# Kernel tuning notes

Hardware: AMD Instinct MI355X
Metric: run time of the kernel (lower is better)

Reference implementation:

```python
import math
import jax, jax.numpy as jnp
import numpy as np

B, N, D, H, L = 8, 1024, 512, 8, 6
HD = D // H
FREQ = 256
K_LORENTZ = 1.0


def lorentz_projx(x, k=K_LORENTZ):
    # geoopt Lorentz.projx: x0 = sqrt(k + ||x_space||^2)
    space = x[..., 1:]
    x0 = jnp.sqrt(k + jnp.sum(space * space, axis=-1, keepdims=True))
    return jnp.concatenate([x0, space], axis=-1)


def layernorm(x, eps=1e-6):
    m = jnp.mean(x, axis=-1, keepdims=True)
    v = jnp.mean((x - m) ** 2, axis=-1, keepdims=True)
    return (x - m) / jnp.sqrt(v + eps)


def make_pe(n, d):
    pos = np.arange(n, dtype=np.float32)[:, None]
    div = np.exp(np.arange(0, d, 2, dtype=np.float32) * (-math.log(10000.0) / d))
    pe = np.zeros((n, d), dtype=np.float32)
    pe[:, 0::2] = np.sin(pos * div)
    pe[:, 1::2] = np.cos(pos * div)
    return jnp.asarray(pe)


def setup_inputs() -> dict:
    key = jax.random.key(0)
    ks = jax.random.split(key, 20)
    s = 0.02
    inp = {
        "t": jax.random.uniform(ks[0], (B,), jnp.float32) * 1000.0,
        "x": jax.random.normal(ks[1], (B, N, D), jnp.float32),
        "mask": jnp.ones((B, N), jnp.float32),
        "pe": make_pe(N, D),
        # timestep embedder MLP (weights stored [in,out])
        "tw1": jax.random.normal(ks[2], (FREQ, D), jnp.float32) * s,
        "tb1": jnp.zeros((D,), jnp.float32),
        "tw2": jax.random.normal(ks[3], (D, D), jnp.float32) * s,
        "tb2": jnp.zeros((D,), jnp.float32),
        # per-layer params stacked over L
        "Wq": jax.random.normal(ks[4], (L, D, D), jnp.float32) * s,
        "bq": jnp.zeros((L, D), jnp.float32),
        "Wk": jax.random.normal(ks[5], (L, D, D), jnp.float32) * s,
        "bk": jnp.zeros((L, D), jnp.float32),
        "Wv": jax.random.normal(ks[6], (L, D, D), jnp.float32) * s,
        "bv": jnp.zeros((L, D), jnp.float32),
        "W1": jax.random.normal(ks[7], (L, D, 4 * D), jnp.float32) * s,
        "b1": jnp.zeros((L, 4 * D), jnp.float32),
        "W2": jax.random.normal(ks[8], (L, 4 * D, D), jnp.float32) * s,
        "b2": jnp.zeros((L, D), jnp.float32),
        "Wada": jax.random.normal(ks[9], (L, D, 6 * D), jnp.float32) * s,
        "bada": jnp.zeros((L, 6 * D), jnp.float32),
    }
    return inp


def timestep_embedding(t, dim=FREQ, max_period=10000.0):
    half = dim // 2
    freqs = jnp.exp(-math.log(max_period) * jnp.arange(half, dtype=jnp.float32) / half)
    args = t[:, None] * freqs[None]
    return jnp.concatenate([jnp.cos(args), jnp.sin(args)], axis=-1)  # [B, dim]


def attention(h, mask, Wq, bq, Wk, bk, Wv, bv):
    # h: [B,N,D], mask: [B,N]
    q = (h @ Wq + bq).reshape(B, N, H, HD).transpose(0, 2, 1, 3)
    k = (h @ Wk + bk).reshape(B, N, H, HD).transpose(0, 2, 1, 3)
    v = (h @ Wv + bv).reshape(B, N, H, HD).transpose(0, 2, 1, 3)
    scores = jnp.einsum("bhqd,bhkd->bhqk", q, k) / math.sqrt(HD)
    # faithful quirk: valid positions get +1 added, invalid get -10000
    mm = jnp.einsum("bi,bj->bij", mask, mask)[:, None]  # [B,1,N,N]
    mm = jnp.where(mm == 0, -10000.0, mm)
    scores = scores + mm
    probs = jax.nn.softmax(scores, axis=-1)
    ctx = jnp.einsum("bhqk,bhkd->bhqd", probs, v)
    return ctx.transpose(0, 2, 1, 3).reshape(B, N, D)


def reference(t, x, mask, pe, tw1, tb1, tw2, tb2, Wq, bq, Wk, bk, Wv, bv,
              W1, b1, W2, b2, Wada, bada):
    # z = x + PositionalEncoding(x) = 2*x + pe
    z = x + (x + pe[None])
    # timestep embedder
    c = timestep_embedding(t) @ tw1 + tb1
    c = jax.nn.silu(c) @ tw2 + tb2  # [B, D]
    for i in range(L):
        ada = jax.nn.silu(c) @ Wada[i] + bada[i]  # [B, 6D]
        sh_msa, sc_msa, g_msa, sh_mlp, sc_mlp, g_mlp = jnp.split(ada, 6, axis=-1)
        h = layernorm(z) * (1.0 + sc_msa[:, None]) + sh_msa[:, None]
        z = z + g_msa[:, None] * attention(h, mask, Wq[i], bq[i], Wk[i], bk[i], Wv[i], bv[i])
        z = lorentz_projx(z)
        h = layernorm(z) * (1.0 + sc_mlp[:, None]) + sh_mlp[:, None]
        m = jax.nn.gelu(h @ W1[i] + b1[i], approximate=True) @ W2[i] + b2[i]
        z = z + g_mlp[:, None] * m
        z = lorentz_projx(z)
    z = lorentz_projx(z)
    return jnp.where(mask[:, :, None] != 0, z, 0.0)
```

## Files before the change

### kernel.cpp

```cpp
#include <hip/hip_runtime.h>
#include <hip/hip_bf16.h>
#include <math.h>

#define NTOK 1024
#define DMODEL 512
#define NHEAD 8
#define HDIM 64
#define BATCH 8
#define NLAYER 6
#define ROWS (BATCH*NTOK)
#define QKVSTR 1536
#define LOG2E 1.44269504f

typedef __attribute__((ext_vector_type(8))) short bf16x8;
typedef __attribute__((ext_vector_type(4))) float f32x4;
typedef unsigned short ushort_t;


__device__ __forceinline__ float silu_f(float x) { return x / (1.f + expf(-x)); }

__device__ __forceinline__ float gelu_tanh_f(float x) {
    float x3 = x * x * x;
    float y2 = 1.5957691216057308f * (x + 0.044715f * x3);
    float e = __builtin_amdgcn_exp2f(-y2 * LOG2E);
    return x / (1.f + e);
}

__device__ __forceinline__ unsigned short f2bf(float x) {
    __hip_bfloat16 b = __float2bfloat16(x);
    return *reinterpret_cast<unsigned short*>(&b);
}

__device__ __forceinline__ float bf2f(unsigned short u) {
    union { float f; unsigned v; } c;
    c.v = (unsigned)u << 16;
    return c.f;
}

template<int NW>
__device__ __forceinline__ float blk_sum(float v, volatile float* scratch) {
    #pragma unroll
    for (int o = 32; o > 0; o >>= 1) v += __shfl_down(v, o);
    if ((threadIdx.x & 63) == 0) scratch[threadIdx.x >> 6] = v;
    __syncthreads();
    float s = scratch[0];
    #pragma unroll
    for (int i = 1; i < NW; i++) s += scratch[i];
    __syncthreads();
    return s;
}


__global__ __launch_bounds__(256) void init_z_kernel(const float* __restrict__ x,
                                                     const float* __restrict__ pe,
                                                     float* __restrict__ z) {
    int i = blockIdx.x * 256 + threadIdx.x;
    const int C4 = DMODEL / 4;
    int row = i / C4;
    int col4 = i - row * C4;
    int n = row & (NTOK - 1);
    float4 xv = ((const float4*)x)[i];
    float4 pv = ((const float4*)pe)[n * C4 + col4];
    float4 o;
    o.x = 2.f * xv.x + pv.x;
    o.y = 2.f * xv.y + pv.y;
    o.z = 2.f * xv.z + pv.z;
    o.w = 2.f * xv.w + pv.w;
    ((float4*)z)[i] = o;
}

__global__ void temb_kernel(const float* __restrict__ t, float* __restrict__ temb) {
    int b = blockIdx.x;
    int j = threadIdx.x;
    float f = expf(-9.210340371976184f * (float)j / 128.f);
    float a = t[b] * f;
    temb[b * 256 + j] = cosf(a);
    temb[b * 256 + 128 + j] = sinf(a);
}

__global__ __launch_bounds__(256) void skinny_part(const float* __restrict__ A,
                                                   const float* __restrict__ W,
                                                   float* __restrict__ part,
                                                   int K, int N, int NL) {
    __shared__ float Als[8][128];
    const int l = blockIdx.z;
    const int n = blockIdx.x * 256 + threadIdx.x;
    const int kc = blockIdx.y;
    const int kbase = kc * 128;
    for (int i = threadIdx.x; i < 8 * 128; i += 256) {
        int b = i >> 7, k = i & 127;
        Als[b][k] = A[b * K + kbase + k];
    }
    __syncthreads();
    float acc[8] = {};
    const float* wp = W + (size_t)l * K * N + (size_t)kbase * N + n;
    for (int k = 0; k < 128; k += 4) {
        float w0 = wp[0];
        float w1 = wp[N];
        float w2 = wp[2 * N];
        float w3 = wp[3 * N];
        wp += 4 * (size_t)N;
        #pragma unroll
        for (int b = 0; b < 8; b++)
            acc[b] += Als[b][k] * w0 + Als[b][k + 1] * w1 + Als[b][k + 2] * w2 + Als[b][k + 3] * w3;
    }
    #pragma unroll
    for (int b = 0; b < 8; b++)
        part[((size_t)kc * 8 + b) * NL + (size_t)l * N + n] = acc[b];
}

template<int ACT>
__global__ __launch_bounds__(256) void skinny_reduce(const float* __restrict__ part,
                                                     const float* __restrict__ bias,
                                                     float* __restrict__ out,
                                                     int KC, int N, int NL) {
    int i = blockIdx.x * 256 + threadIdx.x;
    if (i >= 8 * NL) return;
    int b = i / NL, n = i - b * NL;
    float s = bias[n];
    for (int kc = 0; kc < KC; kc++) s += part[((size_t)kc * 8 + b) * NL + n];
    if (ACT == 1) s = silu_f(s);
    int l = n / N, nl = n - l * N;
    out[((size_t)l * 8 + b) * N + nl] = s;
}

__global__ __launch_bounds__(256) void transp_all(const float* __restrict__ Wq,
                                                  const float* __restrict__ Wk,
                                                  const float* __restrict__ Wv,
                                                  const float* __restrict__ W1,
                                                  const float* __restrict__ W2,
                                                  ushort_t* __restrict__ wqkv_t,
                                                  ushort_t* __restrict__ w1_t,
                                                  ushort_t* __restrict__ w2_t) {
    __shared__ float tile[32][33];
    int blk = blockIdx.x;
    const float* src; ushort_t* dst; int K, N, k0, n0;
    if (blk < 768) {
        int zz = blk >> 8, rem = blk & 255;
        k0 = (rem >> 4) * 32; n0 = (rem & 15) * 32;
        src = zz == 0 ? Wq : (zz == 1 ? Wk : Wv);
        dst = wqkv_t + zz * 512 * 512;
        K = 512; N = 512;
    } else if (blk < 1792) {
        int rem = blk - 768;
        n0 = (rem & 63) * 32; k0 = (rem >> 6) * 32;
        src = W1; dst = w1_t; K = 512; N = 2048;
    } else {
        int rem = blk - 1792;
        n0 = (rem & 15) * 32; k0 = (rem >> 4) * 32;
        src = W2; dst = w2_t; K = 2048; N = 512;
    }
    int c = threadIdx.x & 31, r8 = threadIdx.x >> 5;
    #pragma unroll
    for (int i = 0; i < 4; i++) {
        int r = r8 + i * 8;
        tile[r][c] = src[(size_t)(k0 + r) * N + n0 + c];
    }
    __syncthreads();
    #pragma unroll
    for (int i = 0; i < 4; i++) {
        int rr = r8 + i * 8;
        dst[(size_t)(n0 + rr) * K + k0 + c] = f2bf(tile[c][rr]);
    }
}

__global__ void pack_bias(const float* __restrict__ bq, const float* __restrict__ bk,
                          const float* __restrict__ bv, float* __restrict__ bqkv) {
    int idx = blockIdx.x * 256 + threadIdx.x;
    if (idx >= NLAYER * QKVSTR) return;
    int l = idx / QKVSTR, n = idx - l * QKVSTR;
    float v = (n < 512) ? bq[l * 512 + n] : (n < 1024) ? bk[l * 512 + n - 512] : bv[l * 512 + n - 1024];
    bqkv[idx] = v;
}

template<int ACT, int OUTBF, int QPRESCALE>
__global__ __launch_bounds__(256) void mfma_gemm(const ushort_t* __restrict__ A,
                                                 const ushort_t* __restrict__ Bt,
                                                 const float* __restrict__ bias,
                                                 void* __restrict__ Cout,
                                                 int M, int N, int K) {
    __shared__ ushort_t smem[4 * 128 * 64];
    const int tid = threadIdx.x;
    const int lane = tid & 63, wv = tid >> 6;
    const int wm = (wv >> 1) * 64, wn = (wv & 1) * 64;
    const int lrow = lane & 15, lk = lane >> 4;
    const int m0 = blockIdx.x * 128, n0 = blockIdx.y * 128;
    const int srow = lane >> 3;
    const int qp = lane & 7;
    const int ql = qp ^ srow;

    f32x4 acc[4][4];
    #pragma unroll
    for (int i = 0; i < 4; i++)
        #pragma unroll
        for (int j = 0; j < 4; j++) {
            f32x4 zz = {0.f, 0.f, 0.f, 0.f};
            acc[i][j] = zz;
        }

    const int nK = K >> 6;

    auto STAGE = [&](int p, int ks) {
        const int k0 = ks << 6;
        ushort_t* Ad = smem + p * 8192;
        ushort_t* Bd = smem + 16384 + p * 8192;
        #pragma unroll
        for (int it = 0; it < 4; it++) {
            int chunk = wv * 4 + it;
            int row = chunk * 8 + srow;
            const ushort_t* srcA = A + (size_t)(m0 + row) * K + k0 + ql * 8;
            const ushort_t* srcB = Bt + (size_t)(n0 + row) * K + k0 + ql * 8;
            __builtin_amdgcn_global_load_lds((const __attribute__((address_space(1))) void*)srcA,
                                             (__attribute__((address_space(3))) void*)(Ad + chunk * 512),
                                             16, 0, 0);
            __builtin_amdgcn_global_load_lds((const __attribute__((address_space(1))) void*)srcB,
                                             (__attribute__((address_space(3))) void*)(Bd + chunk * 512),
                                             16, 0, 0);
        }
    };

    STAGE(0, 0);
    int cur = 0;
    for (int ks = 0; ks < nK; ks++) {
        if (ks + 1 < nK) {
            STAGE(cur ^ 1, ks + 1);
            asm volatile("s_waitcnt vmcnt(8)" ::: "memory");
        } else {
            asm volatile("s_waitcnt vmcnt(0)" ::: "memory");
        }
        __builtin_amdgcn_s_barrier();
        asm volatile("" ::: "memory");

        const ushort_t* Ab = smem + cur * 8192;
        const ushort_t* Bb = smem + 16384 + cur * 8192;
        #pragma unroll
        for (int kk = 0; kk < 2; kk++) {
            bf16x8 af[4], bfr[4];
            #pragma unroll
            for (int f = 0; f < 4; f++) {
                int ar = wm + f * 16 + lrow;
                af[f] = *(const bf16x8*)(Ab + ar * 64 + (((kk * 4 + lk) ^ (ar & 7)) << 3));
                int br = wn + f * 16 + lrow;
                bfr[f] = *(const bf16x8*)(Bb + br * 64 + (((kk * 4 + lk) ^ (br & 7)) << 3));
            }
            #pragma unroll
            for (int i = 0; i < 4; i++)
                #pragma unroll
                for (int j = 0; j < 4; j++)
                    acc[i][j] = __builtin_amdgcn_mfma_f32_16x16x32_bf16(af[i], bfr[j], acc[i][j], 0, 0, 0);
        }
        asm volatile("" ::: "memory");
        __builtin_amdgcn_s_barrier();
        cur ^= 1;
    }

    if (OUTBF) {
        __syncthreads();
        #pragma unroll
        for (int j = 0; j < 4; j++) {
            int coll = wn + j * 16 + lrow;
            float bcol = bias[n0 + coll];
            #pragma unroll
            for (int i = 0; i < 4; i++) {
                #pragma unroll
                for (int r = 0; r < 4; r++) {
                    int rowl = wm + i * 16 + lk * 4 + r;
                    float v = acc[i][j][r] + bcol;
                    if (ACT == 1) v = gelu_tanh_f(v);
                    if (QPRESCALE && (n0 + coll) < 512) v *= 0.125f * LOG2E;
                    smem[rowl * 136 + coll] = f2bf(v);
                }
            }
        }
        __syncthreads();
        ushort_t* Co = (ushort_t*)Cout;
        #pragma unroll
        for (int pass = 0; pass < 8; pass++) {
            int rowl = pass * 16 + (tid >> 4);
            int cseg = (tid & 15) * 8;
            uint4 vv = *(const uint4*)(smem + rowl * 136 + cseg);
            *(uint4*)(Co + (size_t)(m0 + rowl) * N + n0 + cseg) = vv;
        }
    } else {
        #pragma unroll
        for (int j = 0; j < 4; j++) {
            int col = n0 + wn + j * 16 + lrow;
            float bcol = bias[col];
            #pragma unroll
            for (int i = 0; i < 4; i++)
                #pragma unroll
                for (int r = 0; r < 4; r++) {
                    int row = m0 + wm + i * 16 + lk * 4 + r;
                    float v = acc[i][j][r] + bcol;
                    if (ACT == 1) v = gelu_tanh_f(v);
                    ((float*)Cout)[(size_t)row * N + col] = v;
                }
        }
    }
}


__global__ __launch_bounds__(128) void ln_mod_kernel(const float* __restrict__ z,
                                                     const float* __restrict__ ada,
                                                     ushort_t* __restrict__ out,
                                                     int sh_off, int sc_off) {
    __shared__ float red[2];
    int row = blockIdx.x;
    int b = row >> 10;
    int tid = threadIdx.x;
    float4 v = ((const float4*)(z + (size_t)row * DMODEL))[tid];
    float s = v.x + v.y + v.z + v.w;
    float mean = blk_sum<2>(s, red) * (1.f / DMODEL);
    float dx = v.x - mean, dy = v.y - mean, dz = v.z - mean, dw = v.w - mean;
    float ssq = dx * dx + dy * dy + dz * dz + dw * dw;
    float var = blk_sum<2>(ssq, red) * (1.f / DMODEL);
    float rstd = rsqrtf(var + 1e-6f);
    const float* ab = ada + b * (6 * DMODEL);
    float4 sc4 = ((const float4*)(ab + sc_off))[tid];
    float4 sh4 = ((const float4*)(ab + sh_off))[tid];
    unsigned short u0 = f2bf(dx * rstd * (1.f + sc4.x) + sh4.x);
    unsigned short u1 = f2bf(dy * rstd * (1.f + sc4.y) + sh4.y);
    unsigned short u2 = f2bf(dz * rstd * (1.f + sc4.z) + sh4.z);
    unsigned short u3 = f2bf(dw * rstd * (1.f + sc4.w) + sh4.w);
    uint2 pk;
    pk.x = (unsigned)u0 | ((unsigned)u1 << 16);
    pk.y = (unsigned)u2 | ((unsigned)u3 << 16);
    ((uint2*)(out + (size_t)row * DMODEL))[tid] = pk;
}

__global__ __launch_bounds__(128) void resid_ln_kernel(float* __restrict__ z,
                                                       const ushort_t* __restrict__ add,
                                                       const float* __restrict__ adaG, int g_off,
                                                       const float* __restrict__ adaLN, int sh_off, int sc_off,
                                                       ushort_t* __restrict__ out) {
    __shared__ float red[2];
    int row = blockIdx.x;
    int b = row >> 10;
    int tid = threadIdx.x;
    float4 v = ((float4*)(z + (size_t)row * DMODEL))[tid];
    uint2 a2 = ((const uint2*)(add + (size_t)row * DMODEL))[tid];
    float4 g4 = ((const float4*)(adaG + b * (6 * DMODEL) + g_off))[tid];
    v.x += g4.x * bf2f((unsigned short)(a2.x & 0xffff));
    v.y += g4.y * bf2f((unsigned short)(a2.x >> 16));
    v.z += g4.z * bf2f((unsigned short)(a2.y & 0xffff));
    v.w += g4.w * bf2f((unsigned short)(a2.y >> 16));
    float ssq = v.x * v.x + v.y * v.y + v.z * v.z + v.w * v.w;
    if (tid == 0) ssq -= v.x * v.x;
    float tot = blk_sum<2>(ssq, red);
    if (tid == 0) v.x = sqrtf(1.f + tot);
    ((float4*)(z + (size_t)row * DMODEL))[tid] = v;
    float s = v.x + v.y + v.z + v.w;
    float mean = blk_sum<2>(s, red) * (1.f / DMODEL);
    float dx = v.x - mean, dy = v.y - mean, dz = v.z - mean, dw = v.w - mean;
    float sq2 = dx * dx + dy * dy + dz * dz + dw * dw;
    float var = blk_sum<2>(sq2, red) * (1.f / DMODEL);
    float rstd = rsqrtf(var + 1e-6f);
    const float* ab = adaLN + b * (6 * DMODEL);
    float4 sc4 = ((const float4*)(ab + sc_off))[tid];
    float4 sh4 = ((const float4*)(ab + sh_off))[tid];
    unsigned short u0 = f2bf(dx * rstd * (1.f + sc4.x) + sh4.x);
    unsigned short u1 = f2bf(dy * rstd * (1.f + sc4.y) + sh4.y);
    unsigned short u2 = f2bf(dz * rstd * (1.f + sc4.z) + sh4.z);
    unsigned short u3 = f2bf(dw * rstd * (1.f + sc4.w) + sh4.w);
    uint2 pk;
    pk.x = (unsigned)u0 | ((unsigned)u1 << 16);
    pk.y = (unsigned)u2 | ((unsigned)u3 << 16);
    ((uint2*)(out + (size_t)row * DMODEL))[tid] = pk;
}

__global__ __launch_bounds__(128) void resid_final_kernel(const float* __restrict__ z,
                                                          const ushort_t* __restrict__ add,
                                                          const float* __restrict__ adaG, int g_off,
                                                          const float* __restrict__ mask,
                                                          float* __restrict__ out) {
    __shared__ float red[2];
    int row = blockIdx.x;
    int b = row >> 10;
    int tid = threadIdx.x;
    float4 v = ((const float4*)(z + (size_t)row * DMODEL))[tid];
    uint2 a2 = ((const uint2*)(add + (size_t)row * DMODEL))[tid];
    float4 g4 = ((const float4*)(adaG + b * (6 * DMODEL) + g_off))[tid];
    v.x += g4.x * bf2f((unsigned short)(a2.x & 0xffff));
    v.y += g4.y * bf2f((unsigned short)(a2.x >> 16));
    v.z += g4.z * bf2f((unsigned short)(a2.y & 0xffff));
    v.w += g4.w * bf2f((unsigned short)(a2.y >> 16));
    float ssq = v.x * v.x + v.y * v.y + v.z * v.z + v.w * v.w;
    if (tid == 0) ssq -= v.x * v.x;
    float tot = blk_sum<2>(ssq, red);
    if (tid == 0) v.x = sqrtf(1.f + tot);
    float m = mask[row];
    if (m == 0.f) { v.x = 0.f; v.y = 0.f; v.z = 0.f; v.w = 0.f; }
    ((float4*)(out + (size_t)row * DMODEL))[tid] = v;
}

__global__ __launch_bounds__(512) void flash_attn_mfma(const ushort_t* __restrict__ qkv,
                                                       const float* __restrict__ mask,
                                                       ushort_t* __restrict__ ctx) {
    __shared__ ushort_t Kls[64 * 64];
    __shared__ ushort_t Vt[64 * 64];
    __shared__ ushort_t Pls[8][16 * 64];
    __shared__ float Mall[NTOK];

    const int tid = threadIdx.x;
    const int lane = tid & 63, w = tid >> 6;
    const int c = lane & 15, g = lane >> 4;
    const int bh = blockIdx.x;
    const int q0 = blockIdx.y * 128;
    const int b = bh >> 3, h = bh & 7;

    const ushort_t* qptr = qkv + (size_t)(b * NTOK + q0 + w * 16 + c) * QKVSTR + h * HDIM + g * 8;
    bf16x8 aq0 = *(const bf16x8*)(qptr);
    bf16x8 aq1 = *(const bf16x8*)(qptr + 32);

    const float mq = mask[b * NTOK + q0 + w * 16 + c];

    #pragma unroll
    for (int i = 0; i < 2; i++) Mall[tid + i * 512] = mask[b * NTOK + tid + i * 512];

    f32x4 o[4];
    #pragma unroll
    for (int j = 0; j < 4; j++) { f32x4 zz = {0.f,0.f,0.f,0.f}; o[j] = zz; }
    float l_run = 0.f;

    const int srow = lane >> 3, qp = lane & 7, ql = qp ^ srow;
    const int kp = tid & 31, dg = tid >> 5;

    char* Pw = (char*)&Pls[w][0];
    const int cswz = (c & 7) << 4;

    for (int kt = 0; kt < NTOK / 64; kt++) {
        const int k0 = kt * 64;
        __syncthreads();
        {
            int row = w * 8 + srow;
            const ushort_t* src = qkv + (size_t)(b * NTOK + k0 + row) * QKVSTR + 512 + h * HDIM + ql * 8;
            __builtin_amdgcn_global_load_lds((const __attribute__((address_space(1))) void*)src,
                                             (__attribute__((address_space(3))) void*)(Kls + w * 512),
                                             16, 0, 0);
        }
        {
            const ushort_t* v0 = qkv + (size_t)(b * NTOK + k0 + 2 * kp) * QKVSTR + 1024 + h * HDIM + dg * 4;
            uint2 r0 = *(const uint2*)v0;
            uint2 r1 = *(const uint2*)(v0 + QKVSTR);
            const ushort_t* e0 = (const ushort_t*)&r0;
            const ushort_t* e1 = (const ushort_t*)&r1;
            unsigned* VtU = (unsigned*)Vt;
            #pragma unroll
            for (int i = 0; i < 4; i++) {
                int d = dg * 4 + i;
                unsigned pk = (unsigned)e0[i] | ((unsigned)e1[i] << 16);
                VtU[d * 32 + (((kp >> 2) ^ (d & 7)) << 2) + (kp & 3)] = pk;
            }
        }
        __syncthreads();

        f32x4 s[4];
        #pragma unroll
        for (int j = 0; j < 4; j++) { f32x4 zz = {0.f,0.f,0.f,0.f}; s[j] = zz; }
        __builtin_amdgcn_s_setprio(1);
        #pragma unroll
        for (int j = 0; j < 4; j++) {
            int row = j * 16 + c;
            bf16x8 ak0 = *(const bf16x8*)(Kls + row * 64 + ((g ^ (row & 7)) << 3));
            bf16x8 ak1 = *(const bf16x8*)(Kls + row * 64 + (((4 + g) ^ (row & 7)) << 3));
            s[j] = __builtin_amdgcn_mfma_f32_16x16x32_bf16(ak0, aq0, s[j], 0, 0, 0);
            s[j] = __builtin_amdgcn_mfma_f32_16x16x32_bf16(ak1, aq1, s[j], 0, 0, 0);
        }
        __builtin_amdgcn_s_setprio(0);

        #pragma unroll
        for (int j = 0; j < 4; j++) {
            float4 mk4 = *(const float4*)&Mall[k0 + j * 16 + 4 * g];
            const float* mkp = (const float*)&mk4;
            float p[4];
            #pragma unroll
            for (int r = 0; r < 4; r++) {
                float mm = mq * mkp[r];
                float sv = s[j][r] + (mm == 0.f ? -14427.0f : mm * LOG2E);
                p[r] = exp2f(sv);
                l_run += p[r];
            }
            uint2 pk2;
            pk2.x = (unsigned)f2bf(p[0]) | ((unsigned)f2bf(p[1]) << 16);
            pk2.y = (unsigned)f2bf(p[2]) | ((unsigned)f2bf(p[3]) << 16);
            *(uint2*)(Pw + c * 128 + ((j * 32 + g * 8) ^ cswz)) = pk2;
        }

        __builtin_amdgcn_s_setprio(1);
        #pragma unroll
        for (int kk = 0; kk < 2; kk++) {
            bf16x8 pa = *(const bf16x8*)(Pw + c * 128 + ((kk * 64 + g * 16) ^ cswz));
            #pragma unroll
            for (int j = 0; j < 4; j++) {
                int vr = j * 16 + c;
                bf16x8 bv = *(const bf16x8*)(Vt + vr * 64 + (((kk * 4 + g) ^ (vr & 7)) << 3));
                o[j] = __builtin_amdgcn_mfma_f32_16x16x32_bf16(pa, bv, o[j], 0, 0, 0);
            }
        }
        __builtin_amdgcn_s_setprio(0);
    }

    l_run += __shfl_xor(l_run, 16);
    l_run += __shfl_xor(l_run, 32);

    float invr[4];
    #pragma unroll
    for (int r = 0; r < 4; r++) invr[r] = 1.f / __shfl(l_run, (g << 4) + 4 * g + r);
    #pragma unroll
    for (int r = 0; r < 4; r++) {
        size_t row = (size_t)(b * NTOK + q0 + w * 16 + 4 * g + r) * DMODEL + h * HDIM;
        #pragma unroll
        for (int j = 0; j < 4; j++)
            ctx[row + j * 16 + c] = f2bf(o[j][r] * invr[r]);
    }
}


extern "C" void kernel_launch(void* const* d_in, const int* in_sizes, int n_in,
                              void* d_out, int out_size, void* d_ws, size_t ws_size,
                              hipStream_t stream) {
    const float* t    = (const float*)d_in[0];
    const float* x    = (const float*)d_in[1];
    const float* mask = (const float*)d_in[2];
    const float* pe   = (const float*)d_in[3];
    const float* tw1  = (const float*)d_in[4];
    const float* tb1  = (const float*)d_in[5];
    const float* tw2  = (const float*)d_in[6];
    const float* tb2  = (const float*)d_in[7];
    const float* Wq   = (const float*)d_in[8];
    const float* bq   = (const float*)d_in[9];
    const float* Wk   = (const float*)d_in[10];
    const float* bk   = (const float*)d_in[11];
    const float* Wv   = (const float*)d_in[12];
    const float* bv   = (const float*)d_in[13];
    const float* W1   = (const float*)d_in[14];
    const float* b1   = (const float*)d_in[15];
    const float* W2   = (const float*)d_in[16];
    const float* b2   = (const float*)d_in[17];
    const float* Wada = (const float*)d_in[18];
    const float* bada = (const float*)d_in[19];
    float* out = (float*)d_out;

    float* z      = (float*)d_ws;
    ushort_t* cxb = (ushort_t*)(z + (size_t)ROWS * DMODEL);
    ushort_t* qkv = cxb + (size_t)ROWS * DMODEL;
    ushort_t* mid = qkv;
    ushort_t* hb  = qkv + (size_t)ROWS * 2048;
    ushort_t* wqkv_t = hb + (size_t)ROWS * DMODEL;
    ushort_t* w1_t   = wqkv_t + 1536 * 512;
    ushort_t* w2_t   = w1_t + 2048 * 512;
    float* bqkv  = (float*)(w2_t + 512 * 2048);
    float* temb  = bqkv + NLAYER * QKVSTR;
    float* cmid  = temb + BATCH * 256;
    float* scs   = cmid + BATCH * DMODEL;
    float* part  = scs + BATCH * DMODEL;
    float* ada_all = part + 4 * 8 * (NLAYER * 3072);

    init_z_kernel<<<ROWS * DMODEL / 4 / 256, 256, 0, stream>>>(x, pe, z);
    temb_kernel<<<BATCH, 128, 0, stream>>>(t, temb);
    pack_bias<<<(NLAYER * QKVSTR + 255) / 256, 256, 0, stream>>>(bq, bk, bv, bqkv);

    skinny_part<<<dim3(2, 2, 1), 256, 0, stream>>>(temb, tw1, part, 256, 512, 512);
    skinny_reduce<1><<<16, 256, 0, stream>>>(part, tb1, cmid, 2, 512, 512);
    skinny_part<<<dim3(2, 4, 1), 256, 0, stream>>>(cmid, tw2, part, 512, 512, 512);
    skinny_reduce<1><<<16, 256, 0, stream>>>(part, tb2, scs, 4, 512, 512);
    skinny_part<<<dim3(12, 4, NLAYER), 256, 0, stream>>>(scs, Wada, part, 512, 3072, NLAYER * 3072);
    skinny_reduce<0><<<(8 * NLAYER * 3072 + 255) / 256, 256, 0, stream>>>(
        part, bada, ada_all, 4, 3072, NLAYER * 3072);

    dim3 gqkv(ROWS / 128, QKVSTR / 128);
    dim3 gmlp1(ROWS / 128, 2048 / 128);
    dim3 gmlp2(ROWS / 128, DMODEL / 128);
    dim3 ga(BATCH * NHEAD, NTOK / 128);

    ln_mod_kernel<<<ROWS, 128, 0, stream>>>(z, ada_all, hb, 0, 512);

    for (int i = 0; i < NLAYER; i++) {
        const float* ada = ada_all + (size_t)i * 8 * 3072;

        transp_all<<<2816, 256, 0, stream>>>(Wq + (size_t)i * 512 * 512,
                                             Wk + (size_t)i * 512 * 512,
                                             Wv + (size_t)i * 512 * 512,
                                             W1 + (size_t)i * 512 * 2048,
                                             W2 + (size_t)i * 2048 * 512,
                                             wqkv_t, w1_t, w2_t);

        mfma_gemm<0, 1, 1><<<gqkv, 256, 0, stream>>>(hb, wqkv_t, bqkv + i * QKVSTR, qkv,
                                                     ROWS, QKVSTR, DMODEL);

        flash_attn_mfma<<<ga, 512, 0, stream>>>(qkv, mask, cxb);

        resid_ln_kernel<<<ROWS, 128, 0, stream>>>(z, cxb, ada, 2 * DMODEL,
                                                  ada, 3 * DMODEL, 4 * DMODEL, hb);

        mfma_gemm<1, 1, 0><<<gmlp1, 256, 0, stream>>>(hb, w1_t, b1 + (size_t)i * 4 * DMODEL, mid,
                                                      ROWS, 4 * DMODEL, DMODEL);
        mfma_gemm<0, 1, 0><<<gmlp2, 256, 0, stream>>>(mid, w2_t, b2 + (size_t)i * DMODEL, cxb,
                                                      ROWS, DMODEL, 4 * DMODEL);

        if (i < NLAYER - 1) {
            const float* adan = ada_all + (size_t)(i + 1) * 8 * 3072;
            resid_ln_kernel<<<ROWS, 128, 0, stream>>>(z, cxb, ada, 5 * DMODEL,
                                                      adan, 0, 512, hb);
        } else {
            resid_final_kernel<<<ROWS, 128, 0, stream>>>(z, cxb, ada, 5 * DMODEL, mask, out);
        }
    }
}
```

Before: 928.6 us.

## Use one wave per row for LN kernels and shrink attention tiles to 64 queries

```diff
diff --git a/kernel.cpp b/kernel.cpp
--- a/kernel.cpp
+++ b/kernel.cpp
@@ -37,17 +37,10 @@
     return c.f;
 }
 
-template<int NW>
-__device__ __forceinline__ float blk_sum(float v, volatile float* scratch) {
-    #pragma unroll
-    for (int o = 32; o > 0; o >>= 1) v += __shfl_down(v, o);
-    if ((threadIdx.x & 63) == 0) scratch[threadIdx.x >> 6] = v;
-    __syncthreads();
-    float s = scratch[0];
-    #pragma unroll
-    for (int i = 1; i < NW; i++) s += scratch[i];
-    __syncthreads();
-    return s;
+__device__ __forceinline__ float wave_sum(float v) {
+    #pragma unroll
+    for (int o = 1; o < 64; o <<= 1) v += __shfl_xor(v, o);
+    return v;
 }
 
 
@@ -300,122 +293,140 @@
 }
 
 
-__global__ __launch_bounds__(128) void ln_mod_kernel(const float* __restrict__ z,
+__global__ __launch_bounds__(256) void ln_mod_kernel(const float* __restrict__ z,
                                                      const float* __restrict__ ada,
                                                      ushort_t* __restrict__ out,
                                                      int sh_off, int sc_off) {
-    __shared__ float red[2];
-    int row = blockIdx.x;
+    int lane = threadIdx.x & 63;
+    int row = blockIdx.x * 4 + (threadIdx.x >> 6);
     int b = row >> 10;
-    int tid = threadIdx.x;
-    float4 v = ((const float4*)(z + (size_t)row * DMODEL))[tid];
-    float s = v.x + v.y + v.z + v.w;
-    float mean = blk_sum<2>(s, red) * (1.f / DMODEL);
-    float dx = v.x - mean, dy = v.y - mean, dz = v.z - mean, dw = v.w - mean;
-    float ssq = dx * dx + dy * dy + dz * dz + dw * dw;
-    float var = blk_sum<2>(ssq, red) * (1.f / DMODEL);
-    float rstd = rsqrtf(var + 1e-6f);
+    const float4* zr = (const float4*)(z + (size_t)row * DMODEL);
+    float4 va = zr[lane * 2], vb = zr[lane * 2 + 1];
+    float s = va.x + va.y + va.z + va.w + vb.x + vb.y + vb.z + vb.w;
+    float mean = wave_sum(s) * (1.f / DMODEL);
+    float d0 = va.x - mean, d1 = va.y - mean, d2 = va.z - mean, d3 = va.w - mean;
+    float d4 = vb.x - mean, d5 = vb.y - mean, d6 = vb.z - mean, d7 = vb.w - mean;
+    float ssq = d0*d0 + d1*d1 + d2*d2 + d3*d3 + d4*d4 + d5*d5 + d6*d6 + d7*d7;
+    float rstd = rsqrtf(wave_sum(ssq) * (1.f / DMODEL) + 1e-6f);
     const float* ab = ada + b * (6 * DMODEL);
-    float4 sc4 = ((const float4*)(ab + sc_off))[tid];
-    float4 sh4 = ((const float4*)(ab + sh_off))[tid];
-    unsigned short u0 = f2bf(dx * rstd * (1.f + sc4.x) + sh4.x);
-    unsigned short u1 = f2bf(dy * rstd * (1.f + sc4.y) + sh4.y);
-    unsigned short u2 = f2bf(dz * rstd * (1.f + sc4.z) + sh4.z);
-    unsigned short u3 = f2bf(dw * rstd * (1.f + sc4.w) + sh4.w);
-    uint2 pk;
-    pk.x = (unsigned)u0 | ((unsigned)u1 << 16);
-    pk.y = (unsigned)u2 | ((unsigned)u3 << 16);
-    ((uint2*)(out + (size_t)row * DMODEL))[tid] = pk;
-}
-
-__global__ __launch_bounds__(128) void resid_ln_kernel(float* __restrict__ z,
+    const float4* scp = (const float4*)(ab + sc_off);
+    const float4* shp = (const float4*)(ab + sh_off);
+    float4 sca = scp[lane * 2], scb = scp[lane * 2 + 1];
+    float4 sha = shp[lane * 2], shb = shp[lane * 2 + 1];
+    uint4 pk;
+    pk.x = (unsigned)f2bf(d0 * rstd * (1.f + sca.x) + sha.x) |
+           ((unsigned)f2bf(d1 * rstd * (1.f + sca.y) + sha.y) << 16);
+    pk.y = (unsigned)f2bf(d2 * rstd * (1.f + sca.z) + sha.z) |
+           ((unsigned)f2bf(d3 * rstd * (1.f + sca.w) + sha.w) << 16);
+    pk.z = (unsigned)f2bf(d4 * rstd * (1.f + scb.x) + shb.x) |
+           ((unsigned)f2bf(d5 * rstd * (1.f + scb.y) + shb.y) << 16);
+    pk.w = (unsigned)f2bf(d6 * rstd * (1.f + scb.z) + shb.z) |
+           ((unsigned)f2bf(d7 * rstd * (1.f + scb.w) + shb.w) << 16);
+    ((uint4*)(out + (size_t)row * DMODEL))[lane] = pk;
+}
+
+__global__ __launch_bounds__(256) void resid_ln_kernel(float* __restrict__ z,
                                                        const ushort_t* __restrict__ add,
                                                        const float* __restrict__ adaG, int g_off,
                                                        const float* __restrict__ adaLN, int sh_off, int sc_off,
                                                        ushort_t* __restrict__ out) {
-    __shared__ float red[2];
-    int row = blockIdx.x;
+    int lane = threadIdx.x & 63;
+    int row = blockIdx.x * 4 + (threadIdx.x >> 6);
     int b = row >> 10;
-    int tid = threadIdx.x;
-    float4 v = ((float4*)(z + (size_t)row * DMODEL))[tid];
-    uint2 a2 = ((const uint2*)(add + (size_t)row * DMODEL))[tid];
-    float4 g4 = ((const float4*)(adaG + b * (6 * DMODEL) + g_off))[tid];
-    v.x += g4.x * bf2f((unsigned short)(a2.x & 0xffff));
-    v.y += g4.y * bf2f((unsigned short)(a2.x >> 16));
-    v.z += g4.z * bf2f((unsigned short)(a2.y & 0xffff));
-    v.w += g4.w * bf2f((unsigned short)(a2.y >> 16));
-    float ssq = v.x * v.x + v.y * v.y + v.z * v.z + v.w * v.w;
-    if (tid == 0) ssq -= v.x * v.x;
-    float tot = blk_sum<2>(ssq, red);
-    if (tid == 0) v.x = sqrtf(1.f + tot);
-    ((float4*)(z + (size_t)row * DMODEL))[tid] = v;
-    float s = v.x + v.y + v.z + v.w;
-    float mean = blk_sum<2>(s, red) * (1.f / DMODEL);
-    float dx = v.x - mean, dy = v.y - mean, dz = v.z - mean, dw = v.w - mean;
-    float sq2 = dx * dx + dy * dy + dz * dz + dw * dw;
-    float var = blk_sum<2>(sq2, red) * (1.f / DMODEL);
-    float rstd = rsqrtf(var + 1e-6f);
+    float4* zr = (float4*)(z + (size_t)row * DMODEL);
+    float4 va = zr[lane * 2], vb = zr[lane * 2 + 1];
+    uint4 a4 = ((const uint4*)(add + (size_t)row * DMODEL))[lane];
+    const float4* gp = (const float4*)(adaG + b * (6 * DMODEL) + g_off);
+    float4 ga = gp[lane * 2], gb = gp[lane * 2 + 1];
+    const ushort_t* e = (const ushort_t*)&a4;
+    va.x += ga.x * bf2f(e[0]); va.y += ga.y * bf2f(e[1]);
+    va.z += ga.z * bf2f(e[2]); va.w += ga.w * bf2f(e[3]);
+    vb.x += gb.x * bf2f(e[4]); vb.y += gb.y * bf2f(e[5]);
+    vb.z += gb.z * bf2f(e[6]); vb.w += gb.w * bf2f(e[7]);
+    float ssq = va.x*va.x + va.y*va.y + va.z*va.z + va.w*va.w
+              + vb.x*vb.x + vb.y*vb.y + vb.z*vb.z + vb.w*vb.w;
+    if (lane == 0) ssq -= va.x * va.x;
+    float tot = wave_sum(ssq);
+    if (lane == 0) va.x = sqrtf(1.f + tot);
+    zr[lane * 2] = va; zr[lane * 2 + 1] = vb;
+    float s = va.x + va.y + va.z + va.w + vb.x + vb.y + vb.z + vb.w;
+    float mean = wave_sum(s) * (1.f / DMODEL);
+    float d0 = va.x - mean, d1 = va.y - mean, d2 = va.z - mean, d3 = va.w - mean;
+    float d4 = vb.x - mean, d5 = vb.y - mean, d6 = vb.z - mean, d7 = vb.w - mean;
+    float sq2 = d0*d0 + d1*d1 + d2*d2 + d3*d3 + d4*d4 + d5*d5 + d6*d6 + d7*d7;
+    float rstd = rsqrtf(wave_sum(sq2) * (1.f / DMODEL) + 1e-6f);
     const float* ab = adaLN + b * (6 * DMODEL);
-    float4 sc4 = ((const float4*)(ab + sc_off))[tid];
-    float4 sh4 = ((const float4*)(ab + sh_off))[tid];
-    unsigned short u0 = f2bf(dx * rstd * (1.f + sc4.x) + sh4.x);
-    unsigned short u1 = f2bf(dy * rstd * (1.f + sc4.y) + sh4.y);
-    unsigned short u2 = f2bf(dz * rstd * (1.f + sc4.z) + sh4.z);
-    unsigned short u3 = f2bf(dw * rstd * (1.f + sc4.w) + sh4.w);
-    uint2 pk;
-    pk.x = (unsigned)u0 | ((unsigned)u1 << 16);
-    pk.y = (unsigned)u2 | ((unsigned)u3 << 16);
-    ((uint2*)(out + (size_t)row * DMODEL))[tid] = pk;
-}
-
-__global__ __launch_bounds__(128) void resid_final_kernel(const float* __restrict__ z,
+    const float4* scp = (const float4*)(ab + sc_off);
+    const float4* shp = (const float4*)(ab + sh_off);
+    float4 sca = scp[lane * 2], scb = scp[lane * 2 + 1];
+    float4 sha = shp[lane * 2], shb = shp[lane * 2 + 1];
+    uint4 pk;
+    pk.x = (unsigned)f2bf(d0 * rstd * (1.f + sca.x) + sha.x) |
+           ((unsigned)f2bf(d1 * rstd * (1.f + sca.y) + sha.y) << 16);
+    pk.y = (unsigned)f2bf(d2 * rstd * (1.f + sca.z) + sha.z) |
+           ((unsigned)f2bf(d3 * rstd * (1.f + sca.w) + sha.w) << 16);
+    pk.z = (unsigned)f2bf(d4 * rstd * (1.f + scb.x) + shb.x) |
+           ((unsigned)f2bf(d5 * rstd * (1.f + scb.y) + shb.y) << 16);
+    pk.w = (unsigned)f2bf(d6 * rstd * (1.f + scb.z) + shb.z) |
+           ((unsigned)f2bf(d7 * rstd * (1.f + scb.w) + shb.w) << 16);
+    ((uint4*)(out + (size_t)row * DMODEL))[lane] = pk;
+}
+
+__global__ __launch_bounds__(256) void resid_final_kernel(const float* __restrict__ z,
                                                           const ushort_t* __restrict__ add,
                                                           const float* __restrict__ adaG, int g_off,
                                                           const float* __restrict__ mask,
                                                           float* __restrict__ out) {
-    __shared__ float red[2];
-    int row = blockIdx.x;
+    int lane = threadIdx.x & 63;
+    int row = blockIdx.x * 4 + (threadIdx.x >> 6);
     int b = row >> 10;
-    int tid = threadIdx.x;
-    float4 v = ((const float4*)(z + (size_t)row * DMODEL))[tid];
-    uint2 a2 = ((const uint2*)(add + (size_t)row * DMODEL))[tid];
-    float4 g4 = ((const float4*)(adaG + b * (6 * DMODEL) + g_off))[tid];
-    v.x += g4.x * bf2f((unsigned short)(a2.x & 0xffff));
-    v.y += g4.y * bf2f((unsigned short)(a2.x >> 16));
-    v.z += g4.z * bf2f((unsigned short)(a2.y & 0xffff));
-    v.w += g4.w * bf2f((unsigned short)(a2.y >> 16));
-    float ssq = v.x * v.x + v.y * v.y + v.z * v.z + v.w * v.w;
-    if (tid == 0) ssq -= v.x * v.x;
-    float tot = blk_sum<2>(ssq, red);
-    if (tid == 0) v.x = sqrtf(1.f + tot);
+    const float4* zr = (const float4*)(z + (size_t)row * DMODEL);
+    float4 va = zr[lane * 2], vb = zr[lane * 2 + 1];
+    uint4 a4 = ((const uint4*)(add + (size_t)row * DMODEL))[lane];
+    const float4* gp = (const float4*)(adaG + b * (6 * DMODEL) + g_off);
+    float4 ga = gp[lane * 2], gb = gp[lane * 2 + 1];
+    const ushort_t* e = (const ushort_t*)&a4;
+    va.x += ga.x * bf2f(e[0]); va.y += ga.y * bf2f(e[1]);
+    va.z += ga.z * bf2f(e[2]); va.w += ga.w * bf2f(e[3]);
+    vb.x += gb.x * bf2f(e[4]); vb.y += gb.y * bf2f(e[5]);
+    vb.z += gb.z * bf2f(e[6]); vb.w += gb.w * bf2f(e[7]);
+    float ssq = va.x*va.x + va.y*va.y + va.z*va.z + va.w*va.w
+              + vb.x*vb.x + vb.y*vb.y + vb.z*vb.z + vb.w*vb.w;
+    if (lane == 0) ssq -= va.x * va.x;
+    float tot = wave_sum(ssq);
+    if (lane == 0) va.x = sqrtf(1.f + tot);
     float m = mask[row];
-    if (m == 0.f) { v.x = 0.f; v.y = 0.f; v.z = 0.f; v.w = 0.f; }
-    ((float4*)(out + (size_t)row * DMODEL))[tid] = v;
-}
-
-__global__ __launch_bounds__(512) void flash_attn_mfma(const ushort_t* __restrict__ qkv,
+    if (m == 0.f) {
+        va.x = va.y = va.z = va.w = 0.f;
+        vb.x = vb.y = vb.z = vb.w = 0.f;
+    }
+    float4* orow = (float4*)(out + (size_t)row * DMODEL);
+    orow[lane * 2] = va; orow[lane * 2 + 1] = vb;
+}
+
+__global__ __launch_bounds__(256) void flash_attn_mfma(const ushort_t* __restrict__ qkv,
                                                        const float* __restrict__ mask,
                                                        ushort_t* __restrict__ ctx) {
     __shared__ ushort_t Kls[64 * 64];
     __shared__ ushort_t Vt[64 * 64];
-    __shared__ ushort_t Pls[8][16 * 64];
+    __shared__ ushort_t Pls[4][16 * 64];
     __shared__ float Mall[NTOK];
 
     const int tid = threadIdx.x;
     const int lane = tid & 63, w = tid >> 6;
     const int c = lane & 15, g = lane >> 4;
     const int bh = blockIdx.x;
-    const int q0 = blockIdx.y * 128;
+    const int q0 = blockIdx.y * 64;
     const int b = bh >> 3, h = bh & 7;
 
     const ushort_t* qptr = qkv + (size_t)(b * NTOK + q0 + w * 16 + c) * QKVSTR + h * HDIM + g * 8;
     bf16x8 aq0 = *(const bf16x8*)(qptr);
     bf16x8 aq1 = *(const bf16x8*)(qptr + 32);
 
-    const float mq = mask[b * NTOK + q0 + w * 16 + c];
-
-    #pragma unroll
-    for (int i = 0; i < 2; i++) Mall[tid + i * 512] = mask[b * NTOK + tid + i * 512];
+    const float mqL = mask[b * NTOK + q0 + w * 16 + c] * LOG2E;
+
+    #pragma unroll
+    for (int i = 0; i < 4; i++) Mall[tid + i * 256] = mask[b * NTOK + tid + i * 256];
 
     f32x4 o[4];
     #pragma unroll
@@ -431,23 +442,25 @@
     for (int kt = 0; kt < NTOK / 64; kt++) {
         const int k0 = kt * 64;
         __syncthreads();
-        {
-            int row = w * 8 + srow;
+        #pragma unroll
+        for (int it = 0; it < 2; it++) {
+            int chunk = w * 2 + it;
+            int row = chunk * 8 + srow;
             const ushort_t* src = qkv + (size_t)(b * NTOK + k0 + row) * QKVSTR + 512 + h * HDIM + ql * 8;
             __builtin_amdgcn_global_load_lds((const __attribute__((address_space(1))) void*)src,
-                                             (__attribute__((address_space(3))) void*)(Kls + w * 512),
+                                             (__attribute__((address_space(3))) void*)(Kls + chunk * 512),
                                              16, 0, 0);
         }
         {
-            const ushort_t* v0 = qkv + (size_t)(b * NTOK + k0 + 2 * kp) * QKVSTR + 1024 + h * HDIM + dg * 4;
-            uint2 r0 = *(const uint2*)v0;
-            uint2 r1 = *(const uint2*)(v0 + QKVSTR);
+            const ushort_t* v0 = qkv + (size_t)(b * NTOK + k0 + 2 * kp) * QKVSTR + 1024 + h * HDIM + dg * 8;
+            uint4 r0 = *(const uint4*)v0;
+            uint4 r1 = *(const uint4*)(v0 + QKVSTR);
             const ushort_t* e0 = (const ushort_t*)&r0;
             const ushort_t* e1 = (const ushort_t*)&r1;
             unsigned* VtU = (unsigned*)Vt;
             #pragma unroll
-            for (int i = 0; i < 4; i++) {
-                int d = dg * 4 + i;
+            for (int i = 0; i < 8; i++) {
+                int d = dg * 8 + i;
                 unsigned pk = (unsigned)e0[i] | ((unsigned)e1[i] << 16);
                 VtU[d * 32 + (((kp >> 2) ^ (d & 7)) << 2) + (kp & 3)] = pk;
             }
@@ -472,17 +485,18 @@
         for (int j = 0; j < 4; j++) {
             float4 mk4 = *(const float4*)&Mall[k0 + j * 16 + 4 * g];
             const float* mkp = (const float*)&mk4;
-            float p[4];
+            unsigned u[4];
             #pragma unroll
             for (int r = 0; r < 4; r++) {
-                float mm = mq * mkp[r];
-                float sv = s[j][r] + (mm == 0.f ? -14427.0f : mm * LOG2E);
-                p[r] = exp2f(sv);
-                l_run += p[r];
+                float v = mqL * mkp[r];
+                float sv = s[j][r] + (v == 0.f ? -14427.0f : v);
+                float p = exp2f(sv);
+                l_run += p;
+                u[r] = __float_as_uint(p);
             }
             uint2 pk2;
-            pk2.x = (unsigned)f2bf(p[0]) | ((unsigned)f2bf(p[1]) << 16);
-            pk2.y = (unsigned)f2bf(p[2]) | ((unsigned)f2bf(p[3]) << 16);
+            pk2.x = (u[0] >> 16) | (u[1] & 0xffff0000u);
+            pk2.y = (u[2] >> 16) | (u[3] & 0xffff0000u);
             *(uint2*)(Pw + c * 128 + ((j * 32 + g * 8) ^ cswz)) = pk2;
         }
 
@@ -571,9 +585,9 @@
     dim3 gqkv(ROWS / 128, QKVSTR / 128);
     dim3 gmlp1(ROWS / 128, 2048 / 128);
     dim3 gmlp2(ROWS / 128, DMODEL / 128);
-    dim3 ga(BATCH * NHEAD, NTOK / 128);
-
-    ln_mod_kernel<<<ROWS, 128, 0, stream>>>(z, ada_all, hb, 0, 512);
+    dim3 ga(BATCH * NHEAD, NTOK / 64);
+
+    ln_mod_kernel<<<ROWS / 4, 256, 0, stream>>>(z, ada_all, hb, 0, 512);
 
     for (int i = 0; i < NLAYER; i++) {
         const float* ada = ada_all + (size_t)i * 8 * 3072;
@@ -588,10 +602,10 @@
         mfma_gemm<0, 1, 1><<<gqkv, 256, 0, stream>>>(hb, wqkv_t, bqkv + i * QKVSTR, qkv,
                                                      ROWS, QKVSTR, DMODEL);
 
-        flash_attn_mfma<<<ga, 512, 0, stream>>>(qkv, mask, cxb);
-
-        resid_ln_kernel<<<ROWS, 128, 0, stream>>>(z, cxb, ada, 2 * DMODEL,
-                                                  ada, 3 * DMODEL, 4 * DMODEL, hb);
+        flash_attn_mfma<<<ga, 256, 0, stream>>>(qkv, mask, cxb);
+
+        resid_ln_kernel<<<ROWS / 4, 256, 0, stream>>>(z, cxb, ada, 2 * DMODEL,
+                                                      ada, 3 * DMODEL, 4 * DMODEL, hb);
 
         mfma_gemm<1, 1, 0><<<gmlp1, 256, 0, stream>>>(hb, w1_t, b1 + (size_t)i * 4 * DMODEL, mid,
                                                       ROWS, 4 * DMODEL, DMODEL);
@@ -600,10 +614,10 @@
 
         if (i < NLAYER - 1) {
             const float* adan = ada_all + (size_t)(i + 1) * 8 * 3072;
-            resid_ln_kernel<<<ROWS, 128, 0, stream>>>(z, cxb, ada, 5 * DMODEL,
-                                                      adan, 0, 512, hb);
+            resid_ln_kernel<<<ROWS / 4, 256, 0, stream>>>(z, cxb, ada, 5 * DMODEL,
+                                                          adan, 0, 512, hb);
         } else {
-            resid_final_kernel<<<ROWS, 128, 0, stream>>>(z, cxb, ada, 5 * DMODEL, mask, out);
-        }
-    }
-}
+            resid_final_kernel<<<ROWS / 4, 256, 0, stream>>>(z, cxb, ada, 5 * DMODEL, mask, out);
+        }
+    }
+}
```

New measurement: 955.5 us. +2.9%, slower.
